# Performance work log

Measured on AMD Instinct MI355X. Metric: run time of the kernel, lower is better.

The kernel has to match this reference:

```python
import jax, jax.numpy as jnp
import numpy as np

K_CLS, M_PROTO, C = 19, 10, 720
EPS_SK, SK_ITERS = 0.05, 3  # standard distributed_sinkhorn defaults (SwAV/ProtoSeg)


def _layernorm(x, g, b, eps=1e-5):
    mu = jnp.mean(x, axis=-1, keepdims=True)
    var = jnp.var(x, axis=-1, keepdims=True)
    return (x - mu) * jax.lax.rsqrt(var + eps) * g + b


def _l2n(x):
    return x / jnp.clip(jnp.linalg.norm(x, axis=-1, keepdims=True), 1e-12, None)


def _masked_sinkhorn(scores, mask):
    # scores: [K, N, M] per-class similarity; mask: [K, N] (1.0 where gt_seg == class k)
    # Faithful to distributed_sinkhorn(init_q) run per class, vectorized over classes
    # with masking instead of data-dependent boolean gather (jit-safe).
    L = jnp.exp(scores / EPS_SK) * mask[..., None]                     # [K, N, M]
    L = L / jnp.clip(jnp.sum(L, axis=(1, 2), keepdims=True), 1e-12, None)
    n = jnp.sum(mask, axis=1)[:, None, None]                           # pixels per class [K,1,1]
    n_safe = jnp.maximum(n, 1.0)

    def body(L, _):
        # normalize each prototype row (sum over pixels), then divide by M
        L = L / jnp.clip(jnp.sum(L, axis=1, keepdims=True), 1e-12, None) / M_PROTO
        # normalize each pixel column (sum over prototypes), then divide by n
        L = L / jnp.clip(jnp.sum(L, axis=2, keepdims=True), 1e-12, None) / n_safe
        L = L * mask[..., None]
        return L, None

    L, _ = jax.lax.scan(body, L, None, length=SK_ITERS)
    return L * n_safe                                                  # [K, N, M]


def setup_inputs() -> dict:
    key = jax.random.key(0)
    k1, k2, k3 = jax.random.split(key, 3)
    N = 4 * 128 * 128  # batch 4, 512x512 crop at HRNet output stride 4
    return {
        "x": jax.random.normal(k1, (N, C), jnp.float32),
        "gt_seg": jax.random.randint(k2, (N,), 0, K_CLS),
        "feat_gamma": jnp.ones((C,), jnp.float32),
        "feat_beta": jnp.zeros((C,), jnp.float32),
        "prototypes": jax.random.normal(k3, (K_CLS, M_PROTO, C), jnp.float32) * 0.02,
    }


def reference(x, gt_seg, feat_gamma, feat_beta, prototypes):
    # similarity_compute (cosine branch)
    xn = _l2n(_layernorm(x, feat_gamma, feat_beta))                    # [N, C]
    protos = _l2n(prototypes)                                          # [K, M, C]
    sim_mat = jnp.einsum('nd,kmd->nmk', xn, protos)                    # [N, M, K]

    # prototype_learning
    s = jnp.max(sim_mat, axis=1)                                       # amax over prototypes -> [N, K]
    pred_seg = jnp.argmax(s, axis=-1)                                  # [N]
    scores = jnp.transpose(sim_mat, (2, 0, 1))                         # [K, N, M]
    mask = jnp.transpose(jax.nn.one_hot(gt_seg, K_CLS, dtype=sim_mat.dtype))  # [K, N]
    q = _masked_sinkhorn(scores, mask)                                 # [K, N, M]
    return sim_mat, q, pred_seg
```

## Files before the change

### kernel.cpp

```cpp
#include <hip/hip_runtime.h>
#include <stdint.h>

#define N_PIX    65536
#define C_DIM    720
#define K_CLS    19
#define M_PROTO  10
#define NPROTO   190
#define CPAD     768
#define OFF_Q    12451840
#define OFF_PRED 24903680

typedef _Float16 half8 __attribute__((ext_vector_type(8)));
typedef _Float16 h4    __attribute__((ext_vector_type(4)));
typedef float    f32x4 __attribute__((ext_vector_type(4)));

#define WS_E       0u
#define WS_G2      768u
#define WS_G3      1536u
#define WS_CNT     2304u
#define WS_TIECNT  2432u
#define WS_PSCALE  4096u
#define WS_EPIX    1052672u
#define WS_U       3674112u
#define WS_TIELIST 3936256u
#define WS_PF16    4198400u
#define WS_PF32    4493312u
#define WS_XH      5046272u

__device__ __forceinline__ void async16(const void* g, void* l) {
    __builtin_amdgcn_global_load_lds(
        (const __attribute__((address_space(1))) unsigned int*)g,
        (__attribute__((address_space(3))) unsigned int*)l, 16, 0, 0);
}

__global__ void zero_acc(float* ws) {
    if (threadIdx.x < 640) ws[threadIdx.x] = 0.f;
}

__global__ void proto_prep(const float* __restrict__ protos,
                           _Float16* __restrict__ pf16,
                           float* __restrict__ pf32) {
    int p = blockIdx.x;
    int tid = threadIdx.x;
    if (p >= NPROTO) {
        for (int c = tid; c < CPAD; c += 256) pf16[(size_t)p * CPAD + c] = (_Float16)0.f;
        return;
    }
    __shared__ float red[256];
    const float* row = protos + (size_t)p * C_DIM;
    float ss = 0.f;
    for (int c = tid; c < C_DIM; c += 256) { float v = row[c]; ss += v * v; }
    red[tid] = ss;
    __syncthreads();
    for (int s = 128; s > 0; s >>= 1) {
        if (tid < s) red[tid] += red[tid + s];
        __syncthreads();
    }
    float invn = 1.f / fmaxf(sqrtf(red[0]), 1e-12f);
    int e8 = p & 7;
    for (int c = tid; c < CPAD; c += 256) {
        float v = (c < C_DIM) ? row[c] * invn : 0.f;
        int sw = (((c >> 3) ^ e8) << 3) | (c & 7);
        pf16[(size_t)p * CPAD + sw] = (_Float16)v;
        if (c < C_DIM) pf32[(size_t)p * C_DIM + c] = v;
    }
}

__global__ __launch_bounds__(256) void stats_xh(const float* __restrict__ x,
                                                const float* __restrict__ gamma,
                                                const float* __restrict__ beta,
                                                float4* __restrict__ pscale,
                                                _Float16* __restrict__ xh) {
    int wave = threadIdx.x >> 6, lane = threadIdx.x & 63;
    int n = blockIdx.x * 4 + wave;
    const float4* row4 = (const float4*)(x + (size_t)n * C_DIM);
    const float4* g4 = (const float4*)gamma;
    const float4* b4 = (const float4*)beta;

    float a[8];
    #pragma unroll
    for (int t = 0; t < 8; ++t) a[t] = 0.f;
    float4 xv[3], gv[3], bv[3];
    #pragma unroll
    for (int j = 0; j < 3; ++j) {
        int f = lane + 64 * j;
        float4 xvv = make_float4(0.f, 0.f, 0.f, 0.f), gvv = xvv, bvv = xvv;
        if (f < 180) { xvv = row4[f]; gvv = g4[f]; bvv = b4[f]; }
        xv[j] = xvv; gv[j] = gvv; bv[j] = bvv;
        #define ACC1(v, g, b) { float g2 = (g)*(g); a[0] += (v); a[1] += (v)*(v); \
            a[2] += (v)*g2; a[3] += (v)*(v)*g2; a[4] += (v)*(g)*(b); a[5] += g2; \
            a[6] += (g)*(b); a[7] += (b)*(b); }
        ACC1(xvv.x, gvv.x, bvv.x); ACC1(xvv.y, gvv.y, bvv.y);
        ACC1(xvv.z, gvv.z, bvv.z); ACC1(xvv.w, gvv.w, bvv.w);
        #undef ACC1
    }
    #pragma unroll
    for (int m = 1; m < 64; m <<= 1) {
        #pragma unroll
        for (int t = 0; t < 8; ++t) a[t] += __shfl_xor(a[t], m);
    }
    float mu   = a[0] * (1.f / 720.f);
    float var  = a[1] * (1.f / 720.f) - mu * mu;
    float rsig = rsqrtf(var + 1e-5f);
    float ny2  = rsig * rsig * (a[3] - 2.f * mu * a[2] + mu * mu * a[5])
               + 2.f * rsig * (a[4] - mu * a[6]) + a[7];
    float rn   = 1.f / fmaxf(sqrtf(fmaxf(ny2, 0.f)), 1e-12f);
    float pp   = rsig * rn;
    float qq   = -pp * mu;
    if (lane == 0) pscale[n] = make_float4(pp, qq, rn, 0.f);

    int e8 = n & 7;
    _Float16* orow = xh + (size_t)n * CPAD;
    #pragma unroll
    for (int j = 0; j < 3; ++j) {
        int f = lane + 64 * j;
        float4 xvv = xv[j], gvv = gv[j], bvv = bv[j];
        h4 o;
        o.x = (_Float16)((pp * xvv.x + qq) * gvv.x + rn * bvv.x);
        o.y = (_Float16)((pp * xvv.y + qq) * gvv.y + rn * bvv.y);
        o.z = (_Float16)((pp * xvv.z + qq) * gvv.z + rn * bvv.z);
        o.w = (_Float16)((pp * xvv.w + qq) * gvv.w + rn * bvv.w);
        int off = ((((f >> 1) ^ e8) << 3) | ((f & 1) << 2));
        *reinterpret_cast<h4*>(orow + off) = o;
    }
}

__global__ __launch_bounds__(256) void gemm_sim(
        const _Float16* __restrict__ xh,
        const _Float16* __restrict__ pf16,
        const int*    __restrict__ gt_seg,
        float* __restrict__ out_sim,
        float* __restrict__ out_pred,
        float* __restrict__ epix,
        float* __restrict__ E,
        float* __restrict__ cnt,
        int*   __restrict__ tiecnt,
        int*   __restrict__ tielist) {
    __shared__ __align__(16) char smem[32768];
    _Float16* xs = (_Float16*)smem;
    _Float16* ps = (_Float16*)(smem + 8192);

    int tid = threadIdx.x;
    int wave = tid >> 6, lane = tid & 63;
    int lane15 = lane & 15, quad = lane >> 4;
    int n0 = blockIdx.x * 64;
    int rsub = lane >> 3, csub = (lane & 7) << 3;

    f32x4 acc[12];
    #pragma unroll
    for (int ct = 0; ct < 12; ++ct)
        acc[ct] = (f32x4){0.f, 0.f, 0.f, 0.f};

    #pragma unroll 1
    for (int ch = 0; ch < 12; ++ch) {
        __syncthreads();
        #pragma unroll
        for (int i = 0; i < 2; ++i) {
            int r0 = wave * 16 + i * 8;
            const _Float16* g = xh + (size_t)(n0 + r0 + rsub) * CPAD + ch * 64 + csub;
            async16(g, xs + r0 * 64);
        }
        #pragma unroll
        for (int i = 0; i < 6; ++i) {
            int r0 = wave * 48 + i * 8;
            const _Float16* g = pf16 + (size_t)(r0 + rsub) * CPAD + ch * 64 + csub;
            async16(g, ps + r0 * 64);
        }
        __syncthreads();
        int e8 = lane15 & 7;
        #pragma unroll
        for (int ks = 0; ks < 2; ++ks) {
            int so = (((ks * 4 + quad) ^ e8) << 3);
            half8 a0 = *reinterpret_cast<const half8*>(xs + (wave * 16 + lane15) * 64 + so);
            half8 b[12];
            #pragma unroll
            for (int ct = 0; ct < 12; ++ct)
                b[ct] = *reinterpret_cast<const half8*>(ps + (ct * 16 + lane15) * 64 + so);
            #pragma unroll
            for (int ct = 0; ct < 12; ++ct)
                acc[ct] = __builtin_amdgcn_mfma_f32_16x16x32_f16(a0, b[ct], acc[ct], 0, 0, 0);
        }
    }

    __syncthreads();
    float* fsm   = (float*)smem;
    float* ebuf  = fsm + wave * 1600;
    float* smaxw = fsm + 6400 + wave * 152;
    float* Eks   = fsm + 7008;
    float* hists = fsm + 7200;
    if (tid < 212) fsm[7008 + tid] = 0.f;
    __syncthreads();

    #pragma unroll
    for (int h = 0; h < 2; ++h) {
        if ((quad >> 1) == h) {
            int prow = (quad - 2 * h) * 4;
            #pragma unroll
            for (int ct = 0; ct < 12; ++ct) {
                int proto = ct * 16 + lane15;
                if (proto < NPROTO) {
                    int kc = proto / 10;
                    int m = proto - kc * 10;
                    int obase = m * 19 + kc;
                    #pragma unroll
                    for (int r = 0; r < 4; ++r)
                        ebuf[(prow + r) * 200 + obase] = acc[ct][r];
                }
            }
        }
        __syncthreads();
        #pragma unroll
        for (int p = 0; p < 8; ++p) {
            int pixel = n0 + wave * 16 + 8 * h + p;
            #pragma unroll
            for (int j = 0; j < 3; ++j) {
                int col = lane + 64 * j;
                if (col < NPROTO)
                    out_sim[(size_t)pixel * 190 + col] = ebuf[p * 200 + col];
            }
        }
        #pragma unroll
        for (int t = lane; t < 152; t += 64) {
            int p = t / 19, k = t - p * 19;
            const float* row = ebuf + p * 200;
            float mx = row[k];
            #pragma unroll
            for (int m = 1; m < 10; ++m) mx = fmaxf(mx, row[m * 19 + k]);
            smaxw[t] = mx;
        }
        __syncthreads();
        if (lane < 8) {
            int p = lane;
            int pixel = n0 + wave * 16 + 8 * h + p;
            float best = smaxw[p * 19], second = -1e30f;
            int bk = 0;
            #pragma unroll
            for (int k = 1; k < 19; ++k) {
                float v = smaxw[p * 19 + k];
                if (v > best) { second = best; best = v; bk = k; }
                else if (v > second) second = v;
            }
            out_pred[pixel] = (float)bk;
            if (best - second < 3e-4f) {
                int pos = atomicAdd(tiecnt, 1);
                if (pos < N_PIX) tielist[pos] = pixel;
            }
            int g = gt_seg[pixel];
            atomicAdd(&hists[g], 1.f);
            const float* row = ebuf + p * 200;
            #pragma unroll
            for (int m = 0; m < 10; ++m) {
                float ev = __expf(row[m * 19 + g] * 20.f);
                epix[(size_t)pixel * 10 + m] = ev;
                atomicAdd(&Eks[g * 10 + m], ev);
            }
        }
        __syncthreads();
    }
    if (tid < 190) atomicAdd(&E[tid], Eks[tid]);
    if (tid < 19)  atomicAdd(&cnt[tid], hists[tid]);
}

__global__ void tiefix(const float* __restrict__ x,
                       const float4* __restrict__ pscale,
                       const float* __restrict__ gamma,
                       const float* __restrict__ beta,
                       const float* __restrict__ pf32,
                       const int* __restrict__ tiecnt,
                       const int* __restrict__ tielist,
                       float* __restrict__ out_pred) {
    __shared__ float xrow[720];
    __shared__ double sd[190];
    int count = *tiecnt;
    if (count > N_PIX) count = N_PIX;
    int wave = threadIdx.x >> 6, lane = threadIdx.x & 63;
    for (int it = blockIdx.x; it < count; it += gridDim.x) {
        int n = tielist[it];
        float4 sc = pscale[n];
        for (int c = threadIdx.x; c < 720; c += 256)
            xrow[c] = (sc.x * x[(size_t)n * 720 + c] + sc.y) * gamma[c] + sc.z * beta[c];
        __syncthreads();
        for (int p = wave; p < NPROTO; p += 4) {
            const float* pr = pf32 + (size_t)p * 720;
            double a = 0.0;
            for (int j = 0; j < 12; ++j) {
                int i = lane + 64 * j;
                if (i < 720) a += (double)xrow[i] * (double)pr[i];
            }
            #pragma unroll
            for (int m = 1; m < 64; m <<= 1) a += __shfl_xor(a, m);
            if (lane == 0) sd[p] = a;
        }
        __syncthreads();
        if (threadIdx.x == 0) {
            double best = -1e300;
            int bk = 0;
            for (int k = 0; k < 19; ++k) {
                double sk = -1e300;
                for (int m = 0; m < 10; ++m) sk = fmax(sk, sd[k * 10 + m]);
                if (sk > best) { best = sk; bk = k; }
            }
            out_pred[n] = (float)bk;
        }
        __syncthreads();
    }
}

__global__ void pk_fused(const float* __restrict__ epix,
                         const int* __restrict__ gt_seg,
                         const float* __restrict__ E,
                         const float* __restrict__ Gprev,
                         const float* __restrict__ cnt,
                         const float* __restrict__ uin,
                         float* __restrict__ uout,
                         float* __restrict__ Gout) {
    __shared__ float Es[190];
    __shared__ float vs[190];
    __shared__ float cs[19];
    __shared__ float Ga[190];
    int tid = threadIdx.x;
    if (tid < 190) { Es[tid] = E[tid]; Ga[tid] = 0.f; }
    if (tid < 19) cs[tid] = cnt[tid];
    __syncthreads();
    if (tid < 190) {
        int k = tid / 10;
        float S = 0.f;
        #pragma unroll
        for (int m = 0; m < 10; ++m) S += Es[k * 10 + m];
        float v0 = 1.f / fmaxf(S, 1e-12f);
        float vv = v0 / (fmaxf(v0 * Es[tid], 1e-12f) * 10.f);
        if (Gprev) vv = vv / (fmaxf(vv * Gprev[tid], 1e-12f) * 10.f);
        vs[tid] = vv;
    }
    __syncthreads();
    int n = blockIdx.x * 256 + tid;
    int g = gt_seg[n];
    float ns = fmaxf(cs[g], 1.f);
    const float* e = epix + (size_t)n * 10;
    float ev[10];
    float dot = 0.f;
    #pragma unroll
    for (int m = 0; m < 10; ++m) { ev[m] = e[m]; dot += ev[m] * vs[g * 10 + m]; }
    float up = uin ? uin[n] : 1.f;
    float c = up * dot;
    float uu = up / (fmaxf(c, 1e-12f) * ns);
    uout[n] = uu;
    #pragma unroll
    for (int m = 0; m < 10; ++m) atomicAdd(&Ga[g * 10 + m], ev[m] * uu);
    __syncthreads();
    if (tid < 190) atomicAdd(&Gout[tid], Ga[tid]);
}

__global__ void p3k_fused(const float* __restrict__ epix,
                          const int* __restrict__ gt_seg,
                          const float* __restrict__ E,
                          const float* __restrict__ G2,
                          const float* __restrict__ G3,
                          const float* __restrict__ cnt,
                          const float* __restrict__ uin,
                          float* __restrict__ qout) {
    __shared__ float Es[190];
    __shared__ float vs[190];
    __shared__ float cs[19];
    int tid = threadIdx.x;
    if (tid < 190) Es[tid] = E[tid];
    if (tid < 19) cs[tid] = cnt[tid];
    __syncthreads();
    if (tid < 190) {
        int k = tid / 10;
        float S = 0.f;
        #pragma unroll
        for (int m = 0; m < 10; ++m) S += Es[k * 10 + m];
        float v0 = 1.f / fmaxf(S, 1e-12f);
        float vv = v0 / (fmaxf(v0 * Es[tid], 1e-12f) * 10.f);
        vv = vv / (fmaxf(vv * G2[tid], 1e-12f) * 10.f);
        vv = vv / (fmaxf(vv * G3[tid], 1e-12f) * 10.f);
        vs[tid] = vv;
    }
    __syncthreads();
    int n = blockIdx.x * 256 + tid;
    int g = gt_seg[n];
    float ns = fmaxf(cs[g], 1.f);
    const float* e = epix + (size_t)n * 10;
    float ev[10];
    float dot = 0.f;
    #pragma unroll
    for (int m = 0; m < 10; ++m) { ev[m] = e[m]; dot += ev[m] * vs[g * 10 + m]; }
    float up = uin[n];
    float c = up * dot;
    float u3 = up / (fmaxf(c, 1e-12f) * ns);
    float2 qv[5];
    #pragma unroll
    for (int j = 0; j < 5; ++j) {
        qv[j].x = ev[2 * j] * u3 * vs[g * 10 + 2 * j] * ns;
        qv[j].y = ev[2 * j + 1] * u3 * vs[g * 10 + 2 * j + 1] * ns;
    }
    const float2 z2 = make_float2(0.f, 0.f);
    for (int k = 0; k < 19; ++k) {
        float2* dst = reinterpret_cast<float2*>(qout + (size_t)k * 655360 + (size_t)n * 10);
        if (k == g) {
            #pragma unroll
            for (int j = 0; j < 5; ++j) dst[j] = qv[j];
        } else {
            #pragma unroll
            for (int j = 0; j < 5; ++j) dst[j] = z2;
        }
    }
}

extern "C" void kernel_launch(void* const* d_in, const int* in_sizes, int n_in,
                              void* d_out, int out_size, void* d_ws, size_t ws_size,
                              hipStream_t stream) {
    const float* x      = (const float*)d_in[0];
    const int*   gt     = (const int*)d_in[1];
    const float* gamma  = (const float*)d_in[2];
    const float* beta   = (const float*)d_in[3];
    const float* protos = (const float*)d_in[4];
    float* out = (float*)d_out;
    char* ws = (char*)d_ws;

    float*  E       = (float*)(ws + WS_E);
    float*  G2      = (float*)(ws + WS_G2);
    float*  G3      = (float*)(ws + WS_G3);
    float*  cnt     = (float*)(ws + WS_CNT);
    int*    tiecnt  = (int*)(ws + WS_TIECNT);
    float4* pscale  = (float4*)(ws + WS_PSCALE);
    float*  epix    = (float*)(ws + WS_EPIX);
    float*  u       = (float*)(ws + WS_U);
    int*    tielist = (int*)(ws + WS_TIELIST);
    _Float16* pf16  = (_Float16*)(ws + WS_PF16);
    float*  pf32    = (float*)(ws + WS_PF32);
    _Float16* xh    = (_Float16*)(ws + WS_XH);

    zero_acc<<<1, 1024, 0, stream>>>((float*)ws);
    proto_prep<<<192, 256, 0, stream>>>(protos, pf16, pf32);
    stats_xh<<<16384, 256, 0, stream>>>(x, gamma, beta, pscale, xh);
    gemm_sim<<<1024, 256, 0, stream>>>(xh, pf16, gt,
                                       out, out + OFF_PRED, epix, E, cnt, tiecnt, tielist);
    tiefix<<<1024, 256, 0, stream>>>(x, pscale, gamma, beta, pf32, tiecnt, tielist, out + OFF_PRED);
    pk_fused<<<256, 256, 0, stream>>>(epix, gt, E, nullptr, cnt, nullptr, u, G2);
    pk_fused<<<256, 256, 0, stream>>>(epix, gt, E, G2, cnt, u, u, G3);
    p3k_fused<<<256, 256, 0, stream>>>(epix, gt, E, G2, G3, cnt, u, out + OFF_Q);
}
```

Measured before the change: 502.7 us.

## Fuse layernorm/normalize stage into GEMM, keeping fp16 rows in LDS

Removes the separate stats_xh kernel and the fp16 xh workspace round-trip. Each GEMM block now reads raw x, computes layernorm and L2 scaling per row, and writes the swizzled fp16 row straight into dynamic LDS. Tiles shrink to 32 pixels with waves split across pixel halves and prototype halves, and the zero_acc launch is folded into proto_prep. In exchange each block uses 72KB of LDS, which lowers occupancy, and the per-row stats loop is serial within each wave.

```diff
diff --git a/kernel.cpp b/kernel.cpp
--- a/kernel.cpp
+++ b/kernel.cpp
@@ -25,7 +25,6 @@
 #define WS_TIELIST 3936256u
 #define WS_PF16    4198400u
 #define WS_PF32    4493312u
-#define WS_XH      5046272u
 
 __device__ __forceinline__ void async16(const void* g, void* l) {
     __builtin_amdgcn_global_load_lds(
@@ -33,17 +32,15 @@
         (__attribute__((address_space(3))) unsigned int*)l, 16, 0, 0);
 }
 
-__global__ void zero_acc(float* ws) {
-    if (threadIdx.x < 640) ws[threadIdx.x] = 0.f;
-}
-
 __global__ void proto_prep(const float* __restrict__ protos,
                            _Float16* __restrict__ pf16,
-                           float* __restrict__ pf32) {
+                           float* __restrict__ pf32,
+                           float* __restrict__ wsf) {
     int p = blockIdx.x;
     int tid = threadIdx.x;
     if (p >= NPROTO) {
         for (int c = tid; c < CPAD; c += 256) pf16[(size_t)p * CPAD + c] = (_Float16)0.f;
+        if (p == 191) for (int i = tid; i < 640; i += 256) wsf[i] = 0.f;
         return;
     }
     __shared__ float red[256];
@@ -66,69 +63,13 @@
     }
 }
 
-__global__ __launch_bounds__(256) void stats_xh(const float* __restrict__ x,
-                                                const float* __restrict__ gamma,
-                                                const float* __restrict__ beta,
-                                                float4* __restrict__ pscale,
-                                                _Float16* __restrict__ xh) {
-    int wave = threadIdx.x >> 6, lane = threadIdx.x & 63;
-    int n = blockIdx.x * 4 + wave;
-    const float4* row4 = (const float4*)(x + (size_t)n * C_DIM);
-    const float4* g4 = (const float4*)gamma;
-    const float4* b4 = (const float4*)beta;
-
-    float a[8];
-    #pragma unroll
-    for (int t = 0; t < 8; ++t) a[t] = 0.f;
-    float4 xv[3], gv[3], bv[3];
-    #pragma unroll
-    for (int j = 0; j < 3; ++j) {
-        int f = lane + 64 * j;
-        float4 xvv = make_float4(0.f, 0.f, 0.f, 0.f), gvv = xvv, bvv = xvv;
-        if (f < 180) { xvv = row4[f]; gvv = g4[f]; bvv = b4[f]; }
-        xv[j] = xvv; gv[j] = gvv; bv[j] = bvv;
-        #define ACC1(v, g, b) { float g2 = (g)*(g); a[0] += (v); a[1] += (v)*(v); \
-            a[2] += (v)*g2; a[3] += (v)*(v)*g2; a[4] += (v)*(g)*(b); a[5] += g2; \
-            a[6] += (g)*(b); a[7] += (b)*(b); }
-        ACC1(xvv.x, gvv.x, bvv.x); ACC1(xvv.y, gvv.y, bvv.y);
-        ACC1(xvv.z, gvv.z, bvv.z); ACC1(xvv.w, gvv.w, bvv.w);
-        #undef ACC1
-    }
-    #pragma unroll
-    for (int m = 1; m < 64; m <<= 1) {
-        #pragma unroll
-        for (int t = 0; t < 8; ++t) a[t] += __shfl_xor(a[t], m);
-    }
-    float mu   = a[0] * (1.f / 720.f);
-    float var  = a[1] * (1.f / 720.f) - mu * mu;
-    float rsig = rsqrtf(var + 1e-5f);
-    float ny2  = rsig * rsig * (a[3] - 2.f * mu * a[2] + mu * mu * a[5])
-               + 2.f * rsig * (a[4] - mu * a[6]) + a[7];
-    float rn   = 1.f / fmaxf(sqrtf(fmaxf(ny2, 0.f)), 1e-12f);
-    float pp   = rsig * rn;
-    float qq   = -pp * mu;
-    if (lane == 0) pscale[n] = make_float4(pp, qq, rn, 0.f);
-
-    int e8 = n & 7;
-    _Float16* orow = xh + (size_t)n * CPAD;
-    #pragma unroll
-    for (int j = 0; j < 3; ++j) {
-        int f = lane + 64 * j;
-        float4 xvv = xv[j], gvv = gv[j], bvv = bv[j];
-        h4 o;
-        o.x = (_Float16)((pp * xvv.x + qq) * gvv.x + rn * bvv.x);
-        o.y = (_Float16)((pp * xvv.y + qq) * gvv.y + rn * bvv.y);
-        o.z = (_Float16)((pp * xvv.z + qq) * gvv.z + rn * bvv.z);
-        o.w = (_Float16)((pp * xvv.w + qq) * gvv.w + rn * bvv.w);
-        int off = ((((f >> 1) ^ e8) << 3) | ((f & 1) << 2));
-        *reinterpret_cast<h4*>(orow + off) = o;
-    }
-}
-
-__global__ __launch_bounds__(256) void gemm_sim(
-        const _Float16* __restrict__ xh,
+__global__ __launch_bounds__(256) void gemm_fused(
+        const float*  __restrict__ x,
+        const float*  __restrict__ gamma,
+        const float*  __restrict__ beta,
         const _Float16* __restrict__ pf16,
         const int*    __restrict__ gt_seg,
+        float4* __restrict__ pscale,
         float* __restrict__ out_sim,
         float* __restrict__ out_pred,
         float* __restrict__ epix,
@@ -136,30 +77,87 @@
         float* __restrict__ cnt,
         int*   __restrict__ tiecnt,
         int*   __restrict__ tielist) {
-    __shared__ __align__(16) char smem[32768];
-    _Float16* xs = (_Float16*)smem;
-    _Float16* ps = (_Float16*)(smem + 8192);
+    extern __shared__ __align__(16) char smem[];
+    _Float16* xt = (_Float16*)smem;
+    _Float16* ps = (_Float16*)(smem + 49152);
 
     int tid = threadIdx.x;
     int wave = tid >> 6, lane = tid & 63;
     int lane15 = lane & 15, quad = lane >> 4;
-    int n0 = blockIdx.x * 64;
+    int n0 = blockIdx.x * 32;
+    int ph = wave & 1, qh = wave >> 1;
     int rsub = lane >> 3, csub = (lane & 7) << 3;
 
-    f32x4 acc[12];
-    #pragma unroll
-    for (int ct = 0; ct < 12; ++ct)
-        acc[ct] = (f32x4){0.f, 0.f, 0.f, 0.f};
-
+    const float4* g4 = (const float4*)gamma;
+    const float4* b4 = (const float4*)beta;
+    float4 gv[3], bv[3];
+    #pragma unroll
+    for (int j = 0; j < 3; ++j) {
+        int f = lane + 64 * j;
+        float4 z = make_float4(0.f, 0.f, 0.f, 0.f);
+        gv[j] = (f < 180) ? g4[f] : z;
+        bv[j] = (f < 180) ? b4[f] : z;
+    }
+    #pragma unroll 1
+    for (int rr = 0; rr < 8; ++rr) {
+        int row = wave * 8 + rr;
+        int n = n0 + row;
+        const float4* row4 = (const float4*)(x + (size_t)n * C_DIM);
+        float a[8];
+        #pragma unroll
+        for (int t = 0; t < 8; ++t) a[t] = 0.f;
+        float4 xv[3];
+        #pragma unroll
+        for (int j = 0; j < 3; ++j) {
+            int f = lane + 64 * j;
+            float4 z = make_float4(0.f, 0.f, 0.f, 0.f);
+            float4 xvv = (f < 180) ? row4[f] : z;
+            xv[j] = xvv;
+            float4 gvv = gv[j], bvv = bv[j];
+            #define ACC1(v, g, b) { float g2 = (g)*(g); a[0] += (v); a[1] += (v)*(v); \
+                a[2] += (v)*g2; a[3] += (v)*(v)*g2; a[4] += (v)*(g)*(b); a[5] += g2; \
+                a[6] += (g)*(b); a[7] += (b)*(b); }
+            ACC1(xvv.x, gvv.x, bvv.x); ACC1(xvv.y, gvv.y, bvv.y);
+            ACC1(xvv.z, gvv.z, bvv.z); ACC1(xvv.w, gvv.w, bvv.w);
+            #undef ACC1
+        }
+        #pragma unroll
+        for (int m = 1; m < 64; m <<= 1) {
+            #pragma unroll
+            for (int t = 0; t < 8; ++t) a[t] += __shfl_xor(a[t], m);
+        }
+        float mu   = a[0] * (1.f / 720.f);
+        float var  = a[1] * (1.f / 720.f) - mu * mu;
+        float rsig = rsqrtf(var + 1e-5f);
+        float ny2  = rsig * rsig * (a[3] - 2.f * mu * a[2] + mu * mu * a[5])
+                   + 2.f * rsig * (a[4] - mu * a[6]) + a[7];
+        float rn   = 1.f / fmaxf(sqrtf(fmaxf(ny2, 0.f)), 1e-12f);
+        float pp   = rsig * rn;
+        float qq   = -pp * mu;
+        if (lane == 0) pscale[n] = make_float4(pp, qq, rn, 0.f);
+        #pragma unroll
+        for (int j = 0; j < 3; ++j) {
+            int f = lane + 64 * j;
+            float4 xvv = xv[j], gvv = gv[j], bvv = bv[j];
+            h4 o;
+            o.x = (_Float16)((pp * xvv.x + qq) * gvv.x + rn * bvv.x);
+            o.y = (_Float16)((pp * xvv.y + qq) * gvv.y + rn * bvv.y);
+            o.z = (_Float16)((pp * xvv.z + qq) * gvv.z + rn * bvv.z);
+            o.w = (_Float16)((pp * xvv.w + qq) * gvv.w + rn * bvv.w);
+            int gl = f >> 1;
+            int gp = (gl & 0x78) | ((gl ^ row) & 7);
+            *reinterpret_cast<h4*>(xt + row * 768 + gp * 8 + (f & 1) * 4) = o;
+        }
+    }
+
+    f32x4 acc[6];
+    #pragma unroll
+    for (int ct = 0; ct < 6; ++ct) acc[ct] = (f32x4){0.f, 0.f, 0.f, 0.f};
+
+    int e8 = lane15 & 7;
     #pragma unroll 1
     for (int ch = 0; ch < 12; ++ch) {
         __syncthreads();
-        #pragma unroll
-        for (int i = 0; i < 2; ++i) {
-            int r0 = wave * 16 + i * 8;
-            const _Float16* g = xh + (size_t)(n0 + r0 + rsub) * CPAD + ch * 64 + csub;
-            async16(g, xs + r0 * 64);
-        }
         #pragma unroll
         for (int i = 0; i < 6; ++i) {
             int r0 = wave * 48 + i * 8;
@@ -167,98 +165,86 @@
             async16(g, ps + r0 * 64);
         }
         __syncthreads();
-        int e8 = lane15 & 7;
         #pragma unroll
         for (int ks = 0; ks < 2; ++ks) {
-            int so = (((ks * 4 + quad) ^ e8) << 3);
-            half8 a0 = *reinterpret_cast<const half8*>(xs + (wave * 16 + lane15) * 64 + so);
-            half8 b[12];
-            #pragma unroll
-            for (int ct = 0; ct < 12; ++ct)
-                b[ct] = *reinterpret_cast<const half8*>(ps + (ct * 16 + lane15) * 64 + so);
-            #pragma unroll
-            for (int ct = 0; ct < 12; ++ct)
+            int s = (ks * 4 + quad) ^ e8;
+            half8 a0 = *reinterpret_cast<const half8*>(
+                xt + (ph * 16 + lane15) * 768 + (ch * 8 + s) * 8);
+            half8 b[6];
+            #pragma unroll
+            for (int ct = 0; ct < 6; ++ct)
+                b[ct] = *reinterpret_cast<const half8*>(
+                    ps + (qh * 96 + ct * 16 + lane15) * 64 + s * 8);
+            #pragma unroll
+            for (int ct = 0; ct < 6; ++ct)
                 acc[ct] = __builtin_amdgcn_mfma_f32_16x16x32_f16(a0, b[ct], acc[ct], 0, 0, 0);
         }
     }
 
     __syncthreads();
     float* fsm   = (float*)smem;
-    float* ebuf  = fsm + wave * 1600;
-    float* smaxw = fsm + 6400 + wave * 152;
+    float* ebuf  = fsm;
+    float* smaxs = fsm + 6400;
     float* Eks   = fsm + 7008;
-    float* hists = fsm + 7200;
-    if (tid < 212) fsm[7008 + tid] = 0.f;
-    __syncthreads();
-
-    #pragma unroll
-    for (int h = 0; h < 2; ++h) {
-        if ((quad >> 1) == h) {
-            int prow = (quad - 2 * h) * 4;
-            #pragma unroll
-            for (int ct = 0; ct < 12; ++ct) {
-                int proto = ct * 16 + lane15;
-                if (proto < NPROTO) {
-                    int kc = proto / 10;
-                    int m = proto - kc * 10;
-                    int obase = m * 19 + kc;
-                    #pragma unroll
-                    for (int r = 0; r < 4; ++r)
-                        ebuf[(prow + r) * 200 + obase] = acc[ct][r];
-                }
-            }
-        }
-        __syncthreads();
-        #pragma unroll
-        for (int p = 0; p < 8; ++p) {
-            int pixel = n0 + wave * 16 + 8 * h + p;
-            #pragma unroll
-            for (int j = 0; j < 3; ++j) {
-                int col = lane + 64 * j;
-                if (col < NPROTO)
-                    out_sim[(size_t)pixel * 190 + col] = ebuf[p * 200 + col];
-            }
-        }
-        #pragma unroll
-        for (int t = lane; t < 152; t += 64) {
-            int p = t / 19, k = t - p * 19;
-            const float* row = ebuf + p * 200;
-            float mx = row[k];
-            #pragma unroll
-            for (int m = 1; m < 10; ++m) mx = fmaxf(mx, row[m * 19 + k]);
-            smaxw[t] = mx;
-        }
-        __syncthreads();
-        if (lane < 8) {
-            int p = lane;
-            int pixel = n0 + wave * 16 + 8 * h + p;
-            float best = smaxw[p * 19], second = -1e30f;
-            int bk = 0;
-            #pragma unroll
-            for (int k = 1; k < 19; ++k) {
-                float v = smaxw[p * 19 + k];
-                if (v > best) { second = best; best = v; bk = k; }
-                else if (v > second) second = v;
-            }
-            out_pred[pixel] = (float)bk;
-            if (best - second < 3e-4f) {
-                int pos = atomicAdd(tiecnt, 1);
-                if (pos < N_PIX) tielist[pos] = pixel;
-            }
-            int g = gt_seg[pixel];
-            atomicAdd(&hists[g], 1.f);
-            const float* row = ebuf + p * 200;
-            #pragma unroll
-            for (int m = 0; m < 10; ++m) {
-                float ev = __expf(row[m * 19 + g] * 20.f);
-                epix[(size_t)pixel * 10 + m] = ev;
-                atomicAdd(&Eks[g * 10 + m], ev);
-            }
-        }
-        __syncthreads();
-    }
+    float* hist  = fsm + 7200;
+    if (tid < 224) fsm[7008 + tid] = 0.f;
+    #pragma unroll
+    for (int ct = 0; ct < 6; ++ct) {
+        int proto = qh * 96 + ct * 16 + lane15;
+        if (proto < NPROTO) {
+            int kc = proto / 10;
+            int m = proto - kc * 10;
+            int ob = m * 19 + kc;
+            int prow = ph * 16 + quad * 4;
+            #pragma unroll
+            for (int r = 0; r < 4; ++r)
+                ebuf[(prow + r) * 200 + ob] = acc[ct][r];
+        }
+    }
+    __syncthreads();
+    for (int t2 = tid; t2 < 32 * 192; t2 += 256) {
+        int p = t2 / 192, col = t2 - p * 192;
+        if (col < NPROTO)
+            out_sim[(size_t)(n0 + p) * 190 + col] = ebuf[p * 200 + col];
+    }
+    for (int t2 = tid; t2 < 608; t2 += 256) {
+        int p = t2 / 19, k = t2 - p * 19;
+        const float* rowp = ebuf + p * 200;
+        float mx = rowp[k];
+        #pragma unroll
+        for (int m = 1; m < 10; ++m) mx = fmaxf(mx, rowp[m * 19 + k]);
+        smaxs[t2] = mx;
+    }
+    __syncthreads();
+    if (tid < 32) {
+        int p = tid;
+        int pixel = n0 + p;
+        float best = smaxs[p * 19], second = -1e30f;
+        int bk = 0;
+        #pragma unroll
+        for (int k = 1; k < 19; ++k) {
+            float v = smaxs[p * 19 + k];
+            if (v > best) { second = best; best = v; bk = k; }
+            else if (v > second) second = v;
+        }
+        out_pred[pixel] = (float)bk;
+        if (best - second < 3e-4f) {
+            int pos = atomicAdd(tiecnt, 1);
+            if (pos < N_PIX) tielist[pos] = pixel;
+        }
+        int g = gt_seg[pixel];
+        atomicAdd(&hist[g], 1.f);
+        const float* rowp = ebuf + p * 200;
+        #pragma unroll
+        for (int m = 0; m < 10; ++m) {
+            float ev = __expf(rowp[m * 19 + g] * 20.f);
+            epix[(size_t)pixel * 10 + m] = ev;
+            atomicAdd(&Eks[g * 10 + m], ev);
+        }
+    }
+    __syncthreads();
     if (tid < 190) atomicAdd(&E[tid], Eks[tid]);
-    if (tid < 19)  atomicAdd(&cnt[tid], hists[tid]);
+    if (tid < 19)  atomicAdd(&cnt[tid], hist[tid]);
 }
 
 __global__ void tiefix(const float* __restrict__ x,
@@ -430,13 +416,18 @@
     int*    tielist = (int*)(ws + WS_TIELIST);
     _Float16* pf16  = (_Float16*)(ws + WS_PF16);
     float*  pf32    = (float*)(ws + WS_PF32);
-    _Float16* xh    = (_Float16*)(ws + WS_XH);
-
-    zero_acc<<<1, 1024, 0, stream>>>((float*)ws);
-    proto_prep<<<192, 256, 0, stream>>>(protos, pf16, pf32);
-    stats_xh<<<16384, 256, 0, stream>>>(x, gamma, beta, pscale, xh);
-    gemm_sim<<<1024, 256, 0, stream>>>(xh, pf16, gt,
-                                       out, out + OFF_PRED, epix, E, cnt, tiecnt, tielist);
+
+    static bool attr_set = false;
+    if (!attr_set) {
+        hipFuncSetAttribute((const void*)gemm_fused,
+                            hipFuncAttributeMaxDynamicSharedMemorySize, 73728);
+        attr_set = true;
+    }
+
+    proto_prep<<<192, 256, 0, stream>>>(protos, pf16, pf32, (float*)ws);
+    gemm_fused<<<2048, 256, 73728, stream>>>(x, gamma, beta, pf16, gt, pscale,
+                                             out, out + OFF_PRED, epix, E, cnt,
+                                             tiecnt, tielist);
     tiefix<<<1024, 256, 0, stream>>>(x, pscale, gamma, beta, pf32, tiecnt, tielist, out + OFF_PRED);
     pk_fused<<<256, 256, 0, stream>>>(epix, gt, E, nullptr, cnt, nullptr, u, G2);
     pk_fused<<<256, 256, 0, stream>>>(epix, gt, E, G2, cnt, u, u, G3);
```

New measurement: 491.0 us. 2.3% less time.
